# Kernel tuning notes

Hardware: AMD Instinct MI355X
Metric: run time of the kernel (lower is better)

## Reference

```python
import math
import jax, jax.numpy as jnp
import numpy as np

N, L, D, H = 2, 2048, 1024, 16
DK = D // H  # 64


def setup_inputs() -> dict:
    key = jax.random.key(0)
    k1, k2, k3, k4, k5 = jax.random.split(key, 5)
    scale = 1.0 / math.sqrt(D)
    return {
        "values": jax.random.normal(k1, (N, L, D), dtype=jnp.float32),
        "keys": jax.random.normal(k2, (N, L, D), dtype=jnp.float32),
        "queries": jax.random.normal(k3, (N, L, D), dtype=jnp.float32),
        "fc_out_w": jax.random.normal(k4, (D, D), dtype=jnp.float32) * scale,
        "fc_out_b": jax.random.normal(k5, (D,), dtype=jnp.float32) * scale,
    }


def reference(values, keys, queries, fc_out_w, fc_out_b):
    n, q_len, _ = queries.shape
    k_len = keys.shape[1]
    v = values.reshape(n, k_len, H, DK)
    k = keys.reshape(n, k_len, H, DK)
    q = queries.reshape(n, q_len, H, DK)
    # NOTE: the original module never applies its per-head Linear layers (dead code),
    # and scales logits AFTER the QK einsum.
    energy = jnp.einsum('nqhd,nkhd->nhqk', q, k)  # [N,H,q,k]
    p_attn = jax.nn.softmax(energy / math.sqrt(DK), axis=3)
    attn = jnp.einsum('nhqk,nkhd->nqhd', p_attn, v).reshape(n, q_len, H * DK)
    # fc_out: torch Linear -> x @ W.T + b
    return attn @ fc_out_w.T + fc_out_b
```

## Files before the change

kernel.cpp:

```cpp
#include <hip/hip_runtime.h>
#include <hip/hip_bf16.h>

#define NBATCH 2
#define SEQ    2048
#define DMODEL 1024
#define NHEAD  16
#define DHEAD  64
#define NHTOT  (NBATCH*NHEAD)

typedef __attribute__((ext_vector_type(8)))  short          short8;
typedef __attribute__((ext_vector_type(4)))  float          f32x4;
typedef __attribute__((ext_vector_type(16))) float          f32x16;
typedef __attribute__((ext_vector_type(4)))  unsigned short ushort4v;

__device__ __forceinline__ unsigned short f2bf(float x) {
  union { __hip_bfloat16 b; unsigned short u; } c;
  c.b = __float2bfloat16(x);
  return c.u;
}

__device__ __forceinline__ unsigned int cvt_pk_bf16(float lo, float hi) {
  unsigned int r;
  asm("v_cvt_pk_bf16_f32 %0, %1, %2" : "=v"(r) : "v"(lo), "v"(hi));
  return r;
}

__device__ __forceinline__ void gl_lds16(const unsigned short* g, unsigned short* l) {
  __builtin_amdgcn_global_load_lds(
      (const __attribute__((address_space(1))) void*)g,
      (__attribute__((address_space(3))) void*)l, 16, 0, 0);
}

__global__ __launch_bounds__(256) void cvt_qk(const float* __restrict__ q,
                                              const float* __restrict__ k,
                                              unsigned short* __restrict__ qb,
                                              unsigned short* __restrict__ kb) {
  const float QSCALE = 0.125f * 1.44269504088896340736f;
  int e = (blockIdx.x * 256 + threadIdx.x) * 4;
  int n = e >> 21;
  int r = e & ((1 << 21) - 1);
  int l = r >> 10;
  int c = r & 1023;
  int h = c >> 6;
  int d = c & 63;
  size_t dst = ((size_t)(n * NHEAD + h) * SEQ + l) * DHEAD + d;
  float4 qv = *reinterpret_cast<const float4*>(q + e);
  float4 kv = *reinterpret_cast<const float4*>(k + e);
  ushort4v qo, ko;
  qo.x = f2bf(qv.x * QSCALE); qo.y = f2bf(qv.y * QSCALE);
  qo.z = f2bf(qv.z * QSCALE); qo.w = f2bf(qv.w * QSCALE);
  ko.x = f2bf(kv.x); ko.y = f2bf(kv.y); ko.z = f2bf(kv.z); ko.w = f2bf(kv.w);
  *reinterpret_cast<ushort4v*>(qb + dst) = qo;
  *reinterpret_cast<ushort4v*>(kb + dst) = ko;
}

__global__ __launch_bounds__(256) void vtrans(const float* __restrict__ v,
                                              unsigned short* __restrict__ vt) {
  __shared__ unsigned short t[64][66];
  int bid = blockIdx.x;
  int nh = bid >> 5;
  int lt = bid & 31;
  int n = nh >> 4, h = nh & 15;
  int lbase = lt * 64;
  #pragma unroll
  for (int j = 0; j < 16; ++j) {
    int e = j * 256 + threadIdx.x;
    int l = e >> 6, d = e & 63;
    float x = v[((size_t)n * SEQ + lbase + l) * DMODEL + h * DHEAD + d];
    t[l][d] = f2bf(x);
  }
  __syncthreads();
  #pragma unroll
  for (int j = 0; j < 16; ++j) {
    int e = j * 256 + threadIdx.x;
    int d = e >> 6, l = e & 63;
    vt[((size_t)nh * DHEAD + d) * SEQ + lbase + l] = t[l][d];
  }
}

__global__ __launch_bounds__(256) void cvt_w(const float* __restrict__ w,
                                             unsigned short* __restrict__ wb) {
  int e = (blockIdx.x * 256 + threadIdx.x) * 4;
  float4 wv = *reinterpret_cast<const float4*>(w + e);
  ushort4v wo;
  wo.x = f2bf(wv.x); wo.y = f2bf(wv.y); wo.z = f2bf(wv.z); wo.w = f2bf(wv.w);
  *reinterpret_cast<ushort4v*>(wb + e) = wo;
}

__global__ __launch_bounds__(512, 2) void attn_fwd(const unsigned short* __restrict__ Qb,
                                                   const unsigned short* __restrict__ Kb,
                                                   const unsigned short* __restrict__ Vt,
                                                   unsigned short* __restrict__ Ab) {
  __shared__ __align__(16) unsigned short kbuf[2][64 * 64];
  __shared__ __align__(16) unsigned short vbuf[2][64 * 64];
  __shared__ __align__(16) unsigned short obuf[4][32][72];

  const int bid = blockIdx.x;
  const int nh = (bid & 7) * 4 + (bid >> 6);
  const int qt = (bid >> 3) & 7;
  const int tid  = threadIdx.x;
  const int wave = tid >> 6;
  const int lane = tid & 63;
  const int l31  = lane & 31;
  const int hi   = lane >> 5;

  const unsigned short* Kb_nh = Kb + (size_t)nh * SEQ * DHEAD;
  const unsigned short* Vt_nh = Vt + (size_t)nh * DHEAD * SEQ;

  const int qglob = qt * 256 + wave * 32 + l31;

  short8 bq[4];
  {
    const unsigned short* Qrow = Qb + ((size_t)nh * SEQ + qglob) * DHEAD + hi * 8;
    #pragma unroll
    for (int ds = 0; ds < 4; ++ds)
      bq[ds] = *reinterpret_cast<const short8*>(Qrow + ds * 16);
  }

  float m_run = -1e30f, l_run = 0.f;
  f32x16 acc[2];
  #pragma unroll
  for (int dt = 0; dt < 2; ++dt)
    #pragma unroll
    for (int r = 0; r < 16; ++r) acc[dt][r] = 0.f;

  auto stage = [&](int buf, int kk) {
    int row = tid >> 3, cs = tid & 7;
    int cg  = cs ^ (row & 7);
    int cb  = tid & 448;
    gl_lds16(Kb_nh + (size_t)(kk + row) * DHEAD + cg * 8, &kbuf[buf][cb * 8]);
    gl_lds16(Vt_nh + (size_t)row * SEQ + kk + cg * 8,     &vbuf[buf][cb * 8]);
  };

  stage(0, 0);
  __syncthreads();

  const int NT = SEQ / 64;
  for (int it = 0; it < NT; ++it) {
    const int cur = it & 1;
    if (it + 1 < NT) stage(cur ^ 1, (it + 1) * 64);

    const unsigned short* kb = kbuf[cur];
    const unsigned short* vb = vbuf[cur];

    f32x16 s[2];
    #pragma unroll
    for (int kt = 0; kt < 2; ++kt) {
      #pragma unroll
      for (int r = 0; r < 16; ++r) s[kt][r] = 0.f;
      const int row = kt * 32 + l31;
      const int sw  = row & 7;
      const unsigned short* kr = kb + row * 64;
      #pragma unroll
      for (int ds = 0; ds < 4; ++ds) {
        short8 ak = *reinterpret_cast<const short8*>(kr + (((ds * 2 + hi) ^ sw) * 8));
        s[kt] = __builtin_amdgcn_mfma_f32_32x32x16_bf16(ak, bq[ds], s[kt], 0, 0, 0);
      }
    }

    float pmax = s[0][0];
    #pragma unroll
    for (int kt = 0; kt < 2; ++kt)
      #pragma unroll
      for (int r = 0; r < 16; ++r) pmax = fmaxf(pmax, s[kt][r]);
    pmax = fmaxf(pmax, __shfl_xor(pmax, 32));

    if (!__all(pmax - m_run <= 8.0f)) {
      float mnew = fmaxf(m_run, pmax);
      float corr = exp2f(m_run - mnew);
      l_run *= corr;
      #pragma unroll
      for (int dt = 0; dt < 2; ++dt)
        #pragma unroll
        for (int r = 0; r < 16; ++r) acc[dt][r] *= corr;
      m_run = mnew;
    }

    float sum = 0.f;
    #pragma unroll
    for (int kt = 0; kt < 2; ++kt)
      #pragma unroll
      for (int r = 0; r < 16; ++r) {
        float p = exp2f(s[kt][r] - m_run);
        s[kt][r] = p;
        sum += p;
      }
    sum += __shfl_xor(sum, 32);
    l_run += sum;

    unsigned int pk[2][8];
    #pragma unroll
    for (int kt = 0; kt < 2; ++kt)
      #pragma unroll
      for (int i = 0; i < 8; ++i)
        pk[kt][i] = cvt_pk_bf16(s[kt][2 * i], s[kt][2 * i + 1]);

    unsigned int pa[4][4];
    #pragma unroll
    for (int ks = 0; ks < 4; ++ks) {
      const int t = ks >> 1, b = (ks & 1) * 4;
      pa[ks][0] = pk[t][b + 0]; pa[ks][2] = pk[t][b + 2];
      asm("v_permlane32_swap_b32 %0, %1" : "+v"(pa[ks][0]), "+v"(pa[ks][2]));
      pa[ks][1] = pk[t][b + 1]; pa[ks][3] = pk[t][b + 3];
      asm("v_permlane32_swap_b32 %0, %1" : "+v"(pa[ks][1]), "+v"(pa[ks][3]));
    }

    #pragma unroll
    for (int dt = 0; dt < 2; ++dt) {
      const int row = dt * 32 + l31;
      const int sw  = row & 7;
      const unsigned short* vr = vb + row * 64;
      #pragma unroll
      for (int ks = 0; ks < 4; ++ks) {
        short8 av = *reinterpret_cast<const short8*>(vr + (((ks * 2 + hi) ^ sw) * 8));
        union { unsigned int u[4]; short8 s8; } pu;
        pu.u[0] = pa[ks][0]; pu.u[1] = pa[ks][1];
        pu.u[2] = pa[ks][2]; pu.u[3] = pa[ks][3];
        acc[dt] = __builtin_amdgcn_mfma_f32_32x32x16_bf16(av, pu.s8, acc[dt], 0, 0, 0);
      }
    }
    __syncthreads();
  }

  const float inv = 1.0f / l_run;
  const int n = nh >> 4, h = nh & 15;
  #pragma unroll
  for (int pass = 0; pass < 2; ++pass) {
    if ((wave >> 2) == pass) {
      const int w = wave & 3;
      #pragma unroll
      for (int dt = 0; dt < 2; ++dt)
        #pragma unroll
        for (int q4 = 0; q4 < 4; ++q4) {
          ushort4v pv;
          pv.x = f2bf(acc[dt][q4 * 4 + 0] * inv);
          pv.y = f2bf(acc[dt][q4 * 4 + 1] * inv);
          pv.z = f2bf(acc[dt][q4 * 4 + 2] * inv);
          pv.w = f2bf(acc[dt][q4 * 4 + 3] * inv);
          *reinterpret_cast<ushort4v*>(&obuf[w][l31][dt * 32 + q4 * 8 + hi * 4]) = pv;
        }
    }
    __syncthreads();
    #pragma unroll
    for (int rep = 0; rep < 2; ++rep) {
      int idx = rep * 512 + tid;
      int qi = idx >> 3, ch = idx & 7;
      int w = qi >> 5, qr = qi & 31;
      short8 vv = *reinterpret_cast<const short8*>(&obuf[w][qr][ch * 8]);
      size_t orow = (size_t)n * SEQ + qt * 256 + pass * 128 + qi;
      *reinterpret_cast<short8*>(Ab + orow * DMODEL + h * 64 + ch * 8) = vv;
    }
    __syncthreads();
  }
}

__global__ __launch_bounds__(256) void fc_gemm(const unsigned short* __restrict__ Ab,
                                               const unsigned short* __restrict__ Wb,
                                               const float* __restrict__ bias,
                                               float* __restrict__ out) {
  __shared__ __align__(16) unsigned short At[2][128 * 32];
  __shared__ __align__(16) unsigned short Bt[2][128 * 32];
  const int bid = blockIdx.x;
  const int bm = bid >> 3;
  const int bn = bid & 7;
  const int tid = threadIdx.x;
  const int wave = tid >> 6, lane = tid & 63;
  const int wr = wave >> 1, wc = wave & 1;
  const int l15 = lane & 15, l4 = lane >> 4;

  f32x4 acc[4][4];
  #pragma unroll
  for (int i = 0; i < 4; ++i)
    #pragma unroll
    for (int j = 0; j < 4; ++j) acc[i][j] = (f32x4){0.f, 0.f, 0.f, 0.f};

  auto stage = [&](int buf, int k0) {
    #pragma unroll
    for (int j = 0; j < 2; ++j) {
      int c = j * 256 + tid;
      int row = c >> 2, cs = c & 3;
      int cg = cs ^ (row & 3);
      int cb = j * 256 + (tid & 192);
      gl_lds16(Ab + (size_t)(bm * 128 + row) * DMODEL + k0 + cg * 8, &At[buf][cb * 8]);
      gl_lds16(Wb + (size_t)(bn * 128 + row) * DMODEL + k0 + cg * 8, &Bt[buf][cb * 8]);
    }
  };

  stage(0, 0);
  __syncthreads();

  const int NT = DMODEL / 32;
  for (int it = 0; it < NT; ++it) {
    int cur = it & 1;
    if (it + 1 < NT) stage(cur ^ 1, (it + 1) * 32);

    short8 af[4], bf[4];
    #pragma unroll
    for (int mt = 0; mt < 4; ++mt) {
      int row = wr * 64 + mt * 16 + l15;
      af[mt] = *reinterpret_cast<const short8*>(&At[cur][row * 32 + ((l4 ^ (l15 & 3)) * 8)]);
    }
    #pragma unroll
    for (int nt = 0; nt < 4; ++nt) {
      int row = wc * 64 + nt * 16 + l15;
      bf[nt] = *reinterpret_cast<const short8*>(&Bt[cur][row * 32 + ((l4 ^ (l15 & 3)) * 8)]);
    }
    #pragma unroll
    for (int mt = 0; mt < 4; ++mt)
      #pragma unroll
      for (int nt = 0; nt < 4; ++nt)
        acc[mt][nt] = __builtin_amdgcn_mfma_f32_16x16x32_bf16(af[mt], bf[nt], acc[mt][nt], 0, 0, 0);
    __syncthreads();
  }

  #pragma unroll
  for (int mt = 0; mt < 4; ++mt)
    #pragma unroll
    for (int nt = 0; nt < 4; ++nt) {
      int col = bn * 128 + wc * 64 + nt * 16 + l15;
      float bv = bias[col];
      #pragma unroll
      for (int r = 0; r < 4; ++r) {
        int row = bm * 128 + wr * 64 + mt * 16 + l4 * 4 + r;
        out[(size_t)row * DMODEL + col] = acc[mt][nt][r] + bv;
      }
    }
}

extern "C" void kernel_launch(void* const* d_in, const int* in_sizes, int n_in,
                              void* d_out, int out_size, void* d_ws, size_t ws_size,
                              hipStream_t stream) {
  const float* values  = (const float*)d_in[0];
  const float* keys    = (const float*)d_in[1];
  const float* queries = (const float*)d_in[2];
  const float* fc_w    = (const float*)d_in[3];
  const float* fc_b    = (const float*)d_in[4];
  float* out = (float*)d_out;

  char* ws = (char*)d_ws;
  const size_t QKV_BYTES = (size_t)NHTOT * SEQ * DHEAD * 2;
  unsigned short* Qb = (unsigned short*)(ws);
  unsigned short* Kb = (unsigned short*)(ws + QKV_BYTES);
  unsigned short* Vt = (unsigned short*)(ws + 2 * QKV_BYTES);
  unsigned short* Wb = (unsigned short*)(ws + 3 * QKV_BYTES);
  unsigned short* Ab = (unsigned short*)(ws + 3 * QKV_BYTES + (size_t)DMODEL * DMODEL * 2);

  cvt_qk<<<4096, 256, 0, stream>>>(queries, keys, Qb, Kb);
  vtrans<<<1024, 256, 0, stream>>>(values, Vt);
  cvt_w<<<1024, 256, 0, stream>>>(fc_w, Wb);
  attn_fwd<<<NHTOT * (SEQ / 256), 512, 0, stream>>>(Qb, Kb, Vt, Ab);
  fc_gemm<<<(NBATCH * SEQ / 128) * (DMODEL / 128), 256, 0, stream>>>(Ab, Wb, fc_b, out);
}
```

Before: 198.3 us.

## Vectorize prep kernels, shrink attention and GEMM tiles, register-staged K/V prefetch

```diff
diff --git a/kernel.cpp b/kernel.cpp
--- a/kernel.cpp
+++ b/kernel.cpp
@@ -36,7 +36,7 @@
                                               unsigned short* __restrict__ qb,
                                               unsigned short* __restrict__ kb) {
   const float QSCALE = 0.125f * 1.44269504088896340736f;
-  int e = (blockIdx.x * 256 + threadIdx.x) * 4;
+  int e = (blockIdx.x * 256 + threadIdx.x) * 8;
   int n = e >> 21;
   int r = e & ((1 << 21) - 1);
   int l = r >> 10;
@@ -44,60 +44,73 @@
   int h = c >> 6;
   int d = c & 63;
   size_t dst = ((size_t)(n * NHEAD + h) * SEQ + l) * DHEAD + d;
-  float4 qv = *reinterpret_cast<const float4*>(q + e);
-  float4 kv = *reinterpret_cast<const float4*>(k + e);
-  ushort4v qo, ko;
-  qo.x = f2bf(qv.x * QSCALE); qo.y = f2bf(qv.y * QSCALE);
-  qo.z = f2bf(qv.z * QSCALE); qo.w = f2bf(qv.w * QSCALE);
-  ko.x = f2bf(kv.x); ko.y = f2bf(kv.y); ko.z = f2bf(kv.z); ko.w = f2bf(kv.w);
-  *reinterpret_cast<ushort4v*>(qb + dst) = qo;
-  *reinterpret_cast<ushort4v*>(kb + dst) = ko;
+  float4 q0 = *reinterpret_cast<const float4*>(q + e);
+  float4 q1 = *reinterpret_cast<const float4*>(q + e + 4);
+  float4 k0 = *reinterpret_cast<const float4*>(k + e);
+  float4 k1 = *reinterpret_cast<const float4*>(k + e + 4);
+  union { unsigned short u[8]; short8 s; } qo, ko;
+  qo.u[0]=f2bf(q0.x*QSCALE); qo.u[1]=f2bf(q0.y*QSCALE);
+  qo.u[2]=f2bf(q0.z*QSCALE); qo.u[3]=f2bf(q0.w*QSCALE);
+  qo.u[4]=f2bf(q1.x*QSCALE); qo.u[5]=f2bf(q1.y*QSCALE);
+  qo.u[6]=f2bf(q1.z*QSCALE); qo.u[7]=f2bf(q1.w*QSCALE);
+  ko.u[0]=f2bf(k0.x); ko.u[1]=f2bf(k0.y); ko.u[2]=f2bf(k0.z); ko.u[3]=f2bf(k0.w);
+  ko.u[4]=f2bf(k1.x); ko.u[5]=f2bf(k1.y); ko.u[6]=f2bf(k1.z); ko.u[7]=f2bf(k1.w);
+  *reinterpret_cast<short8*>(qb + dst) = qo.s;
+  *reinterpret_cast<short8*>(kb + dst) = ko.s;
 }
 
 __global__ __launch_bounds__(256) void vtrans(const float* __restrict__ v,
                                               unsigned short* __restrict__ vt) {
-  __shared__ unsigned short t[64][66];
+  __shared__ __align__(16) unsigned short t[64][76];
   int bid = blockIdx.x;
   int nh = bid >> 5;
   int lt = bid & 31;
   int n = nh >> 4, h = nh & 15;
   int lbase = lt * 64;
   #pragma unroll
-  for (int j = 0; j < 16; ++j) {
-    int e = j * 256 + threadIdx.x;
+  for (int p = 0; p < 4; ++p) {
+    int idx = p * 256 + threadIdx.x;
+    int e = idx * 4;
     int l = e >> 6, d = e & 63;
-    float x = v[((size_t)n * SEQ + lbase + l) * DMODEL + h * DHEAD + d];
-    t[l][d] = f2bf(x);
+    float4 x = *reinterpret_cast<const float4*>(
+        v + ((size_t)n * SEQ + lbase + l) * DMODEL + h * DHEAD + d);
+    ushort4v o;
+    o.x = f2bf(x.x); o.y = f2bf(x.y); o.z = f2bf(x.z); o.w = f2bf(x.w);
+    *reinterpret_cast<ushort4v*>(&t[l][d]) = o;
   }
   __syncthreads();
   #pragma unroll
-  for (int j = 0; j < 16; ++j) {
-    int e = j * 256 + threadIdx.x;
-    int d = e >> 6, l = e & 63;
-    vt[((size_t)nh * DHEAD + d) * SEQ + lbase + l] = t[l][d];
+  for (int p = 0; p < 4; ++p) {
+    int idx = p * 256 + threadIdx.x;
+    int d = idx >> 4, lq = (idx & 15) * 4;
+    ushort4v o;
+    o.x = t[lq + 0][d]; o.y = t[lq + 1][d];
+    o.z = t[lq + 2][d]; o.w = t[lq + 3][d];
+    *reinterpret_cast<ushort4v*>(
+        vt + ((size_t)nh * DHEAD + d) * SEQ + lbase + lq) = o;
   }
 }
 
 __global__ __launch_bounds__(256) void cvt_w(const float* __restrict__ w,
                                              unsigned short* __restrict__ wb) {
-  int e = (blockIdx.x * 256 + threadIdx.x) * 4;
-  float4 wv = *reinterpret_cast<const float4*>(w + e);
-  ushort4v wo;
-  wo.x = f2bf(wv.x); wo.y = f2bf(wv.y); wo.z = f2bf(wv.z); wo.w = f2bf(wv.w);
-  *reinterpret_cast<ushort4v*>(wb + e) = wo;
-}
-
-__global__ __launch_bounds__(512, 2) void attn_fwd(const unsigned short* __restrict__ Qb,
+  int e = (blockIdx.x * 256 + threadIdx.x) * 8;
+  float4 w0 = *reinterpret_cast<const float4*>(w + e);
+  float4 w1 = *reinterpret_cast<const float4*>(w + e + 4);
+  union { unsigned short u[8]; short8 s; } wo;
+  wo.u[0]=f2bf(w0.x); wo.u[1]=f2bf(w0.y); wo.u[2]=f2bf(w0.z); wo.u[3]=f2bf(w0.w);
+  wo.u[4]=f2bf(w1.x); wo.u[5]=f2bf(w1.y); wo.u[6]=f2bf(w1.z); wo.u[7]=f2bf(w1.w);
+  *reinterpret_cast<short8*>(wb + e) = wo.s;
+}
+
+__global__ __launch_bounds__(256, 2) void attn_fwd(const unsigned short* __restrict__ Qb,
                                                    const unsigned short* __restrict__ Kb,
                                                    const unsigned short* __restrict__ Vt,
                                                    unsigned short* __restrict__ Ab) {
-  __shared__ __align__(16) unsigned short kbuf[2][64 * 64];
-  __shared__ __align__(16) unsigned short vbuf[2][64 * 64];
-  __shared__ __align__(16) unsigned short obuf[4][32][72];
+  __shared__ __align__(16) unsigned short smem[4 * 4096];
 
   const int bid = blockIdx.x;
-  const int nh = (bid & 7) * 4 + (bid >> 6);
-  const int qt = (bid >> 3) & 7;
+  const int nh = (bid & 7) * 4 + (bid >> 7);
+  const int qt = (bid >> 3) & 15;
   const int tid  = threadIdx.x;
   const int wave = tid >> 6;
   const int lane = tid & 63;
@@ -107,7 +120,7 @@
   const unsigned short* Kb_nh = Kb + (size_t)nh * SEQ * DHEAD;
   const unsigned short* Vt_nh = Vt + (size_t)nh * DHEAD * SEQ;
 
-  const int qglob = qt * 256 + wave * 32 + l31;
+  const int qglob = qt * 128 + wave * 32 + l31;
 
   short8 bq[4];
   {
@@ -124,26 +137,44 @@
     #pragma unroll
     for (int r = 0; r < 16; ++r) acc[dt][r] = 0.f;
 
-  auto stage = [&](int buf, int kk) {
-    int row = tid >> 3, cs = tid & 7;
-    int cg  = cs ^ (row & 7);
-    int cb  = tid & 448;
-    gl_lds16(Kb_nh + (size_t)(kk + row) * DHEAD + cg * 8, &kbuf[buf][cb * 8]);
-    gl_lds16(Vt_nh + (size_t)row * SEQ + kk + cg * 8,     &vbuf[buf][cb * 8]);
+  int4 kreg[2], vreg[2];
+  auto stage_load = [&](int kk) {
+    #pragma unroll
+    for (int j = 0; j < 2; ++j) {
+      int c = j * 256 + tid;
+      int row = c >> 3, cs = c & 7;
+      kreg[j] = *reinterpret_cast<const int4*>(Kb_nh + (size_t)(kk + row) * DHEAD + cs * 8);
+      vreg[j] = *reinterpret_cast<const int4*>(Vt_nh + (size_t)row * SEQ + kk + cs * 8);
+    }
   };
-
-  stage(0, 0);
+  auto stage_write = [&](int buf) {
+    unsigned short* kd = smem + buf * 4096;
+    unsigned short* vd = smem + 2 * 4096 + buf * 4096;
+    #pragma unroll
+    for (int j = 0; j < 2; ++j) {
+      int c = j * 256 + tid;
+      int row = c >> 3, cs = c & 7;
+      int dc = cs ^ (row & 7);
+      *reinterpret_cast<int4*>(kd + (row * 8 + dc) * 8) = kreg[j];
+      *reinterpret_cast<int4*>(vd + (row * 8 + dc) * 8) = vreg[j];
+    }
+  };
+
+  stage_load(0);
+  stage_write(0);
   __syncthreads();
 
   const int NT = SEQ / 64;
   for (int it = 0; it < NT; ++it) {
     const int cur = it & 1;
-    if (it + 1 < NT) stage(cur ^ 1, (it + 1) * 64);
-
-    const unsigned short* kb = kbuf[cur];
-    const unsigned short* vb = vbuf[cur];
+    const bool pf = (it + 1 < NT);
+    if (pf) stage_load((it + 1) * 64);
+
+    const unsigned short* kb = smem + cur * 4096;
+    const unsigned short* vb = smem + 2 * 4096 + cur * 4096;
 
     f32x16 s[2];
+    __builtin_amdgcn_s_setprio(1);
     #pragma unroll
     for (int kt = 0; kt < 2; ++kt) {
       #pragma unroll
@@ -157,6 +188,7 @@
         s[kt] = __builtin_amdgcn_mfma_f32_32x32x16_bf16(ak, bq[ds], s[kt], 0, 0, 0);
       }
     }
+    __builtin_amdgcn_s_setprio(0);
 
     float pmax = s[0][0];
     #pragma unroll
@@ -205,6 +237,9 @@
       asm("v_permlane32_swap_b32 %0, %1" : "+v"(pa[ks][1]), "+v"(pa[ks][3]));
     }
 
+    if (pf) stage_write(cur ^ 1);
+
+    __builtin_amdgcn_s_setprio(1);
     #pragma unroll
     for (int dt = 0; dt < 2; ++dt) {
       const int row = dt * 32 + l31;
@@ -219,109 +254,111 @@
         acc[dt] = __builtin_amdgcn_mfma_f32_32x32x16_bf16(av, pu.s8, acc[dt], 0, 0, 0);
       }
     }
+    __builtin_amdgcn_s_setprio(0);
     __syncthreads();
   }
 
+  unsigned short (*obuf)[32][76] = (unsigned short(*)[32][76])(&smem[0]);
   const float inv = 1.0f / l_run;
   const int n = nh >> 4, h = nh & 15;
   #pragma unroll
-  for (int pass = 0; pass < 2; ++pass) {
-    if ((wave >> 2) == pass) {
-      const int w = wave & 3;
-      #pragma unroll
-      for (int dt = 0; dt < 2; ++dt)
-        #pragma unroll
-        for (int q4 = 0; q4 < 4; ++q4) {
-          ushort4v pv;
-          pv.x = f2bf(acc[dt][q4 * 4 + 0] * inv);
-          pv.y = f2bf(acc[dt][q4 * 4 + 1] * inv);
-          pv.z = f2bf(acc[dt][q4 * 4 + 2] * inv);
-          pv.w = f2bf(acc[dt][q4 * 4 + 3] * inv);
-          *reinterpret_cast<ushort4v*>(&obuf[w][l31][dt * 32 + q4 * 8 + hi * 4]) = pv;
-        }
-    }
-    __syncthreads();
-    #pragma unroll
-    for (int rep = 0; rep < 2; ++rep) {
-      int idx = rep * 512 + tid;
-      int qi = idx >> 3, ch = idx & 7;
-      int w = qi >> 5, qr = qi & 31;
-      short8 vv = *reinterpret_cast<const short8*>(&obuf[w][qr][ch * 8]);
-      size_t orow = (size_t)n * SEQ + qt * 256 + pass * 128 + qi;
-      *reinterpret_cast<short8*>(Ab + orow * DMODEL + h * 64 + ch * 8) = vv;
-    }
-    __syncthreads();
-  }
-}
-
-__global__ __launch_bounds__(256) void fc_gemm(const unsigned short* __restrict__ Ab,
-                                               const unsigned short* __restrict__ Wb,
-                                               const float* __restrict__ bias,
-                                               float* __restrict__ out) {
-  __shared__ __align__(16) unsigned short At[2][128 * 32];
-  __shared__ __align__(16) unsigned short Bt[2][128 * 32];
+  for (int dt = 0; dt < 2; ++dt)
+    #pragma unroll
+    for (int q4 = 0; q4 < 4; ++q4) {
+      ushort4v pv;
+      pv.x = f2bf(acc[dt][q4 * 4 + 0] * inv);
+      pv.y = f2bf(acc[dt][q4 * 4 + 1] * inv);
+      pv.z = f2bf(acc[dt][q4 * 4 + 2] * inv);
+      pv.w = f2bf(acc[dt][q4 * 4 + 3] * inv);
+      *reinterpret_cast<ushort4v*>(&obuf[wave][l31][dt * 32 + q4 * 8 + hi * 4]) = pv;
+    }
+  __syncthreads();
+  #pragma unroll
+  for (int rep = 0; rep < 4; ++rep) {
+    int idx = rep * 256 + tid;
+    int qi = idx >> 3, ch = idx & 7;
+    int w = qi >> 5, qr = qi & 31;
+    union { unsigned short u[8]; short8 s; } vv;
+    #pragma unroll
+    for (int i = 0; i < 8; ++i) vv.u[i] = obuf[w][qr][ch * 8 + i];
+    size_t orow = (size_t)n * SEQ + qt * 128 + qi;
+    *reinterpret_cast<short8*>(Ab + orow * DMODEL + h * 64 + ch * 8) = vv.s;
+  }
+}
+
+__global__ __launch_bounds__(256, 4) void fc_gemm(const unsigned short* __restrict__ Ab,
+                                                  const unsigned short* __restrict__ Wb,
+                                                  const float* __restrict__ bias,
+                                                  float* __restrict__ out) {
+  __shared__ __align__(16) unsigned short At[2][64 * 64];
+  __shared__ __align__(16) unsigned short Bt[2][64 * 64];
   const int bid = blockIdx.x;
-  const int bm = bid >> 3;
-  const int bn = bid & 7;
+  const int bn = (bid & 7) * 2 + ((bid >> 3) & 1);
+  const int bm = bid >> 4;
   const int tid = threadIdx.x;
   const int wave = tid >> 6, lane = tid & 63;
   const int wr = wave >> 1, wc = wave & 1;
   const int l15 = lane & 15, l4 = lane >> 4;
 
-  f32x4 acc[4][4];
-  #pragma unroll
-  for (int i = 0; i < 4; ++i)
-    #pragma unroll
-    for (int j = 0; j < 4; ++j) acc[i][j] = (f32x4){0.f, 0.f, 0.f, 0.f};
+  f32x4 acc[2][2];
+  #pragma unroll
+  for (int i = 0; i < 2; ++i)
+    #pragma unroll
+    for (int j = 0; j < 2; ++j) acc[i][j] = (f32x4){0.f, 0.f, 0.f, 0.f};
 
   auto stage = [&](int buf, int k0) {
     #pragma unroll
     for (int j = 0; j < 2; ++j) {
       int c = j * 256 + tid;
-      int row = c >> 2, cs = c & 3;
-      int cg = cs ^ (row & 3);
+      int row = c >> 3, cs = c & 7;
+      int cg = cs ^ (row & 7);
       int cb = j * 256 + (tid & 192);
-      gl_lds16(Ab + (size_t)(bm * 128 + row) * DMODEL + k0 + cg * 8, &At[buf][cb * 8]);
-      gl_lds16(Wb + (size_t)(bn * 128 + row) * DMODEL + k0 + cg * 8, &Bt[buf][cb * 8]);
+      gl_lds16(Ab + (size_t)(bm * 64 + row) * DMODEL + k0 + cg * 8, &At[buf][cb * 8]);
+      gl_lds16(Wb + (size_t)(bn * 64 + row) * DMODEL + k0 + cg * 8, &Bt[buf][cb * 8]);
     }
   };
 
   stage(0, 0);
   __syncthreads();
 
-  const int NT = DMODEL / 32;
+  const int NT = DMODEL / 64;
   for (int it = 0; it < NT; ++it) {
     int cur = it & 1;
-    if (it + 1 < NT) stage(cur ^ 1, (it + 1) * 32);
-
-    short8 af[4], bf[4];
-    #pragma unroll
-    for (int mt = 0; mt < 4; ++mt) {
-      int row = wr * 64 + mt * 16 + l15;
-      af[mt] = *reinterpret_cast<const short8*>(&At[cur][row * 32 + ((l4 ^ (l15 & 3)) * 8)]);
-    }
-    #pragma unroll
-    for (int nt = 0; nt < 4; ++nt) {
-      int row = wc * 64 + nt * 16 + l15;
-      bf[nt] = *reinterpret_cast<const short8*>(&Bt[cur][row * 32 + ((l4 ^ (l15 & 3)) * 8)]);
-    }
-    #pragma unroll
-    for (int mt = 0; mt < 4; ++mt)
-      #pragma unroll
-      for (int nt = 0; nt < 4; ++nt)
-        acc[mt][nt] = __builtin_amdgcn_mfma_f32_16x16x32_bf16(af[mt], bf[nt], acc[mt][nt], 0, 0, 0);
+    if (it + 1 < NT) stage(cur ^ 1, (it + 1) * 64);
+
+    #pragma unroll
+    for (int s = 0; s < 2; ++s) {
+      short8 af[2], bf2[2];
+      #pragma unroll
+      for (int mt = 0; mt < 2; ++mt) {
+        int row = wr * 32 + mt * 16 + l15;
+        af[mt] = *reinterpret_cast<const short8*>(
+            &At[cur][row * 64 + (((s * 4 + l4) ^ (row & 7)) * 8)]);
+      }
+      #pragma unroll
+      for (int nt = 0; nt < 2; ++nt) {
+        int row = wc * 32 + nt * 16 + l15;
+        bf2[nt] = *reinterpret_cast<const short8*>(
+            &Bt[cur][row * 64 + (((s * 4 + l4) ^ (row & 7)) * 8)]);
+      }
+      #pragma unroll
+      for (int mt = 0; mt < 2; ++mt)
+        #pragma unroll
+        for (int nt = 0; nt < 2; ++nt)
+          acc[mt][nt] = __builtin_amdgcn_mfma_f32_16x16x32_bf16(af[mt], bf2[nt], acc[mt][nt], 0, 0, 0);
+    }
     __syncthreads();
   }
 
   #pragma unroll
-  for (int mt = 0; mt < 4; ++mt)
-    #pragma unroll
-    for (int nt = 0; nt < 4; ++nt) {
-      int col = bn * 128 + wc * 64 + nt * 16 + l15;
+  for (int mt = 0; mt < 2; ++mt)
+    #pragma unroll
+    for (int nt = 0; nt < 2; ++nt) {
+      int col = bn * 64 + wc * 32 + nt * 16 + l15;
       float bv = bias[col];
       #pragma unroll
       for (int r = 0; r < 4; ++r) {
-        int row = bm * 128 + wr * 64 + mt * 16 + l4 * 4 + r;
+        int row = bm * 64 + wr * 32 + mt * 16 + l4 * 4 + r;
         out[(size_t)row * DMODEL + col] = acc[mt][nt][r] + bv;
       }
     }
@@ -345,9 +382,9 @@
   unsigned short* Wb = (unsigned short*)(ws + 3 * QKV_BYTES);
   unsigned short* Ab = (unsigned short*)(ws + 3 * QKV_BYTES + (size_t)DMODEL * DMODEL * 2);
 
-  cvt_qk<<<4096, 256, 0, stream>>>(queries, keys, Qb, Kb);
+  cvt_qk<<<2048, 256, 0, stream>>>(queries, keys, Qb, Kb);
   vtrans<<<1024, 256, 0, stream>>>(values, Vt);
-  cvt_w<<<1024, 256, 0, stream>>>(fc_w, Wb);
-  attn_fwd<<<NHTOT * (SEQ / 256), 512, 0, stream>>>(Qb, Kb, Vt, Ab);
-  fc_gemm<<<(NBATCH * SEQ / 128) * (DMODEL / 128), 256, 0, stream>>>(Ab, Wb, fc_b, out);
-}
+  cvt_w<<<512, 256, 0, stream>>>(fc_w, Wb);
+  attn_fwd<<<NHTOT * (SEQ / 128), 256, 0, stream>>>(Qb, Kb, Vt, Ab);
+  fc_gemm<<<(NBATCH * SEQ / 64) * (DMODEL / 64), 256, 0, stream>>>(Ab, Wb, fc_b, out);
+}
```

Result: slower. 206.5 us (+4.2%).
